# Kernel optimization log

Measured on AMD Instinct MI355X. Metric: run time of the kernel, lower is better.

## Reference

```python
import jax, jax.numpy as jnp
import numpy as np

NUM_EXPERTS = 4
TOPK = 1
TEMPERATURE = 1.0
NORM_TOPK_PROB = True
N_CLS = 1
N_REL = 4


def setup_inputs() -> dict:
    key = jax.random.key(0)
    ks = jax.random.split(key, 7)
    B, N_total, D, r, E = 64, 1029, 768, 64, NUM_EXPERTS
    x = jax.random.normal(ks[0], (B, N_total, D), dtype=jnp.float32)
    # parameters (torch Linear convention: weight [out, in])
    Wd = jax.random.normal(ks[1], (r, D), dtype=jnp.float32) * (1.0 / np.sqrt(D))
    Wg = jax.random.normal(ks[2], (E, r), dtype=jnp.float32) * (1.0 / np.sqrt(r))
    We = jax.random.normal(ks[3], (E, r, r), dtype=jnp.float32) * (1.0 / np.sqrt(r))
    be = jax.random.normal(ks[4], (E, r), dtype=jnp.float32) * 0.01
    Wu = jax.random.normal(ks[5], (D, r), dtype=jnp.float32) * (1.0 / np.sqrt(r))
    gamma = jnp.ones((D,), dtype=jnp.float32)  # LayerScale init_values=1.0
    return {"x": x, "Wd": Wd, "Wg": Wg, "We": We, "be": be, "Wu": Wu, "gamma": gamma}


def reference(x, Wd, Wg, We, be, Wu, gamma):
    # proj_down (bias=False) + exact GELU (nn.GELU default)
    h = jax.nn.gelu(jnp.einsum('bnd,rd->bnr', x, Wd), approximate=False)  # [B,Nt,r]
    cls_tok = h[:, :N_CLS, :]
    rel_tok = h[:, N_CLS:N_CLS + N_REL, :]
    t = h[:, N_CLS + N_REL:, :]                                           # [B,N,r]
    B, N, r = t.shape

    # gating: softmax scores, top-k selection
    logits = jnp.einsum('bnr,er->bne', t, Wg) / TEMPERATURE
    scores = jax.nn.softmax(logits, axis=-1)                              # [B,N,E]
    topk_w, topk_idx = jax.lax.top_k(scores, TOPK)                        # [B,N,K]
    if TOPK > 1 and NORM_TOPK_PROB:
        topk_w = topk_w / jnp.sum(topk_w, axis=-1, keepdims=True)

    # experts are tiny Linear(r,r): compute all experts densely, then gather.
    # Same math as per-expert gather/GEMM/scatter-combine in the source.
    expert_all = jnp.einsum('bnr,esr->bnes', t, We) + be                  # [B,N,E,r]
    idx_b = jnp.broadcast_to(topk_idx[..., None], (B, N, TOPK, r))
    sel = jnp.take_along_axis(expert_all, idx_b, axis=2)                  # [B,N,K,r]
    combine = jnp.sum(sel * topk_w[..., None], axis=2)                    # [B,N,r]

    full = jnp.concatenate([cls_tok, rel_tok, t + combine], axis=1)       # [B,Nt,r]
    # proj_up (bias=False) + LayerScale
    return jnp.einsum('bnr,dr->bnd', full, Wu) * gamma
```

## Files before the change

kernel.cpp:

```cpp
#include <hip/hip_runtime.h>
#include <math.h>


#define GELU(v) (0.5f*(v)*(1.0f + erff((v)*0.70710678118654752440f)))

__global__ __launch_bounds__(256) void k1_proj_gelu(
    const float* __restrict__ x, const float* __restrict__ Wd,
    float* __restrict__ h)
{
    __shared__ float As[64][68];
    __shared__ float Bs[64][68];
    const int tid = threadIdx.x;
    const int bm  = blockIdx.x;
    const int tm4 = (tid >> 4) << 2;
    const int tn4 = (tid & 15) << 2;
    const float* xblk = x + (size_t)bm * 64 * 768;

    float acc[4][4];
    #pragma unroll
    for (int i = 0; i < 4; ++i)
        #pragma unroll
        for (int j = 0; j < 4; ++j) acc[i][j] = 0.f;

    for (int kt = 0; kt < 768; kt += 64) {
        #pragma unroll
        for (int p = 0; p < 4; ++p) {
            int li = p*1024 + tid*4;
            int m = li >> 6, k = li & 63;
            float4 v = *(const float4*)(xblk + m*768 + kt + k);
            *(float4*)&As[m][k] = v;
        }
        #pragma unroll
        for (int p = 0; p < 4; ++p) {
            int li = p*1024 + tid*4;
            int j = li >> 6, k = li & 63;
            float4 v = *(const float4*)(Wd + j*768 + kt + k);
            int c = j ^ (((k >> 2) & 7) << 2);
            Bs[k+0][c] = v.x; Bs[k+1][c] = v.y; Bs[k+2][c] = v.z; Bs[k+3][c] = v.w;
        }
        __syncthreads();
        #pragma unroll
        for (int kk = 0; kk < 64; kk += 4) {
            const int swz = ((kk >> 2) & 7) << 2;
            float4 av[4], bv[4];
            #pragma unroll
            for (int i = 0; i < 4; ++i) av[i] = *(const float4*)&As[tm4 + i][kk];
            #pragma unroll
            for (int r = 0; r < 4; ++r) bv[r] = *(const float4*)&Bs[kk + r][tn4 ^ swz];
            #pragma unroll
            for (int i = 0; i < 4; ++i) {
                acc[i][0] += av[i].x*bv[0].x; acc[i][1] += av[i].x*bv[0].y;
                acc[i][2] += av[i].x*bv[0].z; acc[i][3] += av[i].x*bv[0].w;
                acc[i][0] += av[i].y*bv[1].x; acc[i][1] += av[i].y*bv[1].y;
                acc[i][2] += av[i].y*bv[1].z; acc[i][3] += av[i].y*bv[1].w;
                acc[i][0] += av[i].z*bv[2].x; acc[i][1] += av[i].z*bv[2].y;
                acc[i][2] += av[i].z*bv[2].z; acc[i][3] += av[i].z*bv[2].w;
                acc[i][0] += av[i].w*bv[3].x; acc[i][1] += av[i].w*bv[3].y;
                acc[i][2] += av[i].w*bv[3].z; acc[i][3] += av[i].w*bv[3].w;
            }
        }
        __syncthreads();
    }
    #pragma unroll
    for (int i = 0; i < 4; ++i) {
        int token = bm*64 + tm4 + i;
        float4 o;
        o.x = GELU(acc[i][0]); o.y = GELU(acc[i][1]);
        o.z = GELU(acc[i][2]); o.w = GELU(acc[i][3]);
        *(float4*)(h + (size_t)token*64 + tn4) = o;
    }
}

__global__ __launch_bounds__(256) void k2_moe(
    const float* __restrict__ Wg, const float* __restrict__ We,
    const float* __restrict__ be, float* __restrict__ h)
{
    __shared__ float sWg[4*64];
    __shared__ float sBe[4*64];
    __shared__ float sWeT[4*64*65];
    __shared__ float sT[4][64];
    const int tid = threadIdx.x;

    for (int i = tid; i < 4*64; i += 256) { sWg[i] = Wg[i]; sBe[i] = be[i]; }
    for (int i = tid; i < 4*64*64; i += 256) {
        int e = i >> 12, rem = i & 4095, s = rem >> 6, k = rem & 63;
        sWeT[(e*64 + k)*65 + s] = We[i];
    }
    __syncthreads();

    const int wv = tid >> 6, lane = tid & 63;
    #pragma unroll 1
    for (int it = 0; it < 16; ++it) {
        int mt = blockIdx.x*64 + wv*16 + it;
        int b = mt >> 10, n = mt & 1023;
        int token = b*1029 + 5 + n;
        float t = h[(size_t)token*64 + lane];

        float l0 = t * sWg[      lane];
        float l1 = t * sWg[ 64 + lane];
        float l2 = t * sWg[128 + lane];
        float l3 = t * sWg[192 + lane];
        #pragma unroll
        for (int off = 32; off > 0; off >>= 1) {
            l0 += __shfl_xor(l0, off);
            l1 += __shfl_xor(l1, off);
            l2 += __shfl_xor(l2, off);
            l3 += __shfl_xor(l3, off);
        }
        int ei = 0; float lm = l0;
        if (l1 > lm) { lm = l1; ei = 1; }
        if (l2 > lm) { lm = l2; ei = 2; }
        if (l3 > lm) { lm = l3; ei = 3; }
        float s = expf(l0 - lm) + expf(l1 - lm) + expf(l2 - lm) + expf(l3 - lm);
        float w = 1.0f / s;

        sT[wv][lane] = t;
        float o = sBe[ei*64 + lane];
        const float* wp = &sWeT[(ei*64)*65 + lane];
        #pragma unroll 8
        for (int k = 0; k < 64; ++k)
            o += sT[wv][k] * wp[k*65];

        h[(size_t)token*64 + lane] = t + w * o;
    }
}

__global__ __launch_bounds__(256) void k3_up_gamma(
    const float* __restrict__ h, const float* __restrict__ Wu,
    const float* __restrict__ gamma, float* __restrict__ out)
{
    __shared__ float Fs[64][68];
    __shared__ float Ws[64][132];
    const int tid = threadIdx.x;
    const int bm = blockIdx.x, bn = blockIdx.y;
    const int tm4 = (tid >> 4) << 2;
    const int tn8 = (tid & 15) << 3;

    #pragma unroll
    for (int p = 0; p < 4; ++p) {
        int li = p*1024 + tid*4;
        int m = li >> 6, k = li & 63;
        *(float4*)&Fs[m][k] = *(const float4*)(h + (size_t)(bm*64 + m)*64 + k);
    }
    #pragma unroll
    for (int p = 0; p < 8; ++p) {
        int li = p*1024 + tid*4;
        int dl = li >> 6, k = li & 63;
        float4 v = *(const float4*)(Wu + (size_t)(bn*128 + dl)*64 + k);
        int c = dl ^ (((k >> 2) & 7) << 2);
        Ws[k+0][c] = v.x; Ws[k+1][c] = v.y; Ws[k+2][c] = v.z; Ws[k+3][c] = v.w;
    }
    __syncthreads();

    float acc[4][8];
    #pragma unroll
    for (int i = 0; i < 4; ++i)
        #pragma unroll
        for (int j = 0; j < 8; ++j) acc[i][j] = 0.f;

    #pragma unroll
    for (int kk = 0; kk < 64; kk += 4) {
        const int swz = ((kk >> 2) & 7) << 2;
        float4 av[4], blo[4], bhi[4];
        #pragma unroll
        for (int i = 0; i < 4; ++i) av[i] = *(const float4*)&Fs[tm4 + i][kk];
        #pragma unroll
        for (int r = 0; r < 4; ++r) {
            blo[r] = *(const float4*)&Ws[kk + r][ tn8      ^ swz];
            bhi[r] = *(const float4*)&Ws[kk + r][(tn8 + 4) ^ swz];
        }
        #pragma unroll
        for (int i = 0; i < 4; ++i) {
            float a0 = av[i].x, a1 = av[i].y, a2 = av[i].z, a3 = av[i].w;
            acc[i][0] += a0*blo[0].x; acc[i][1] += a0*blo[0].y; acc[i][2] += a0*blo[0].z; acc[i][3] += a0*blo[0].w;
            acc[i][4] += a0*bhi[0].x; acc[i][5] += a0*bhi[0].y; acc[i][6] += a0*bhi[0].z; acc[i][7] += a0*bhi[0].w;
            acc[i][0] += a1*blo[1].x; acc[i][1] += a1*blo[1].y; acc[i][2] += a1*blo[1].z; acc[i][3] += a1*blo[1].w;
            acc[i][4] += a1*bhi[1].x; acc[i][5] += a1*bhi[1].y; acc[i][6] += a1*bhi[1].z; acc[i][7] += a1*bhi[1].w;
            acc[i][0] += a2*blo[2].x; acc[i][1] += a2*blo[2].y; acc[i][2] += a2*blo[2].z; acc[i][3] += a2*blo[2].w;
            acc[i][4] += a2*bhi[2].x; acc[i][5] += a2*bhi[2].y; acc[i][6] += a2*bhi[2].z; acc[i][7] += a2*bhi[2].w;
            acc[i][0] += a3*blo[3].x; acc[i][1] += a3*blo[3].y; acc[i][2] += a3*blo[3].z; acc[i][3] += a3*blo[3].w;
            acc[i][4] += a3*bhi[3].x; acc[i][5] += a3*bhi[3].y; acc[i][6] += a3*bhi[3].z; acc[i][7] += a3*bhi[3].w;
        }
    }

    float4 g0 = *(const float4*)(gamma + bn*128 + tn8);
    float4 g1 = *(const float4*)(gamma + bn*128 + tn8 + 4);
    #pragma unroll
    for (int i = 0; i < 4; ++i) {
        int token = bm*64 + tm4 + i;
        float4 o0, o1;
        o0.x = acc[i][0]*g0.x; o0.y = acc[i][1]*g0.y; o0.z = acc[i][2]*g0.z; o0.w = acc[i][3]*g0.w;
        o1.x = acc[i][4]*g1.x; o1.y = acc[i][5]*g1.y; o1.z = acc[i][6]*g1.z; o1.w = acc[i][7]*g1.w;
        float* op = out + (size_t)token*768 + bn*128 + tn8;
        *(float4*)op       = o0;
        *(float4*)(op + 4) = o1;
    }
}

extern "C" void kernel_launch(void* const* d_in, const int* in_sizes, int n_in,
                              void* d_out, int out_size, void* d_ws, size_t ws_size,
                              hipStream_t stream) {
    const float* x     = (const float*)d_in[0];
    const float* Wd    = (const float*)d_in[1];
    const float* Wg    = (const float*)d_in[2];
    const float* We    = (const float*)d_in[3];
    const float* be    = (const float*)d_in[4];
    const float* Wu    = (const float*)d_in[5];
    const float* gamma = (const float*)d_in[6];
    float* out = (float*)d_out;
    float* h   = (float*)d_ws;

    k1_proj_gelu<<<1029, 256, 0, stream>>>(x, Wd, h);
    k2_moe<<<1024, 256, 0, stream>>>(Wg, We, be, h);
    k3_up_gamma<<<dim3(1029, 6), 256, 0, stream>>>(h, Wu, gamma, out);
}
```

Before: 530.7 us.

## Fuse MoE and up-projection into one bf16 MFMA kernel, double-buffer down-projection

The MoE expert stage and the up-projection now run in a single kernel per 64-token tile. Expert and up-projection weights are pre-converted to bf16 and multiplied with MFMA instructions, so the intermediate no longer makes a second round trip through global memory. The down-projection kernel switches to a 32-wide K tile with register prefetch of the next tile and a higher occupancy hint. Using bf16 for the expert and up-projection matmuls lowers precision versus the fp32 reference. Computing all four experts densely and then selecting one adds MFMA work.

```diff
diff --git a/kernel.cpp b/kernel.cpp
--- a/kernel.cpp
+++ b/kernel.cpp
@@ -4,12 +4,28 @@
 
 #define GELU(v) (0.5f*(v)*(1.0f + erff((v)*0.70710678118654752440f)))
 
-__global__ __launch_bounds__(256) void k1_proj_gelu(
+typedef __attribute__((ext_vector_type(8))) short short8;
+typedef __attribute__((ext_vector_type(4))) float f32x4;
+
+__device__ __forceinline__ short f2bf(float f) {
+    union { float f; unsigned u; } c; c.f = f;
+    unsigned u = c.u;
+    return (short)((u + 0x7fffu + ((u >> 16) & 1u)) >> 16);
+}
+
+__global__ void k0_prep(const float* __restrict__ We, const float* __restrict__ Wu,
+                        short* __restrict__ WeB, short* __restrict__ WuB) {
+    int i = blockIdx.x * 256 + threadIdx.x;
+    if (i < 16384)       WeB[i] = f2bf(We[i]);
+    else if (i < 65536)  WuB[i - 16384] = f2bf(Wu[i - 16384]);
+}
+
+__global__ __launch_bounds__(256, 6) void k1_proj_gelu(
     const float* __restrict__ x, const float* __restrict__ Wd,
     float* __restrict__ h)
 {
-    __shared__ float As[64][68];
-    __shared__ float Bs[64][68];
+    __shared__ float As[64][36];
+    __shared__ float Bs[32][68];
     const int tid = threadIdx.x;
     const int bm  = blockIdx.x;
     const int tm4 = (tid >> 4) << 2;
@@ -22,31 +38,38 @@
         #pragma unroll
         for (int j = 0; j < 4; ++j) acc[i][j] = 0.f;
 
-    for (int kt = 0; kt < 768; kt += 64) {
-        #pragma unroll
-        for (int p = 0; p < 4; ++p) {
-            int li = p*1024 + tid*4;
-            int m = li >> 6, k = li & 63;
-            float4 v = *(const float4*)(xblk + m*768 + kt + k);
-            *(float4*)&As[m][k] = v;
-        }
-        #pragma unroll
-        for (int p = 0; p < 4; ++p) {
-            int li = p*1024 + tid*4;
-            int j = li >> 6, k = li & 63;
-            float4 v = *(const float4*)(Wd + j*768 + kt + k);
-            int c = j ^ (((k >> 2) & 7) << 2);
-            Bs[k+0][c] = v.x; Bs[k+1][c] = v.y; Bs[k+2][c] = v.z; Bs[k+3][c] = v.w;
-        }
-        __syncthreads();
-        #pragma unroll
-        for (int kk = 0; kk < 64; kk += 4) {
+    #pragma unroll
+    for (int p = 0; p < 2; ++p) {
+        int li = p*1024 + tid*4;
+        int m = li >> 5, k = li & 31;
+        *(f32x4*)&As[m][k] = *(const f32x4*)(xblk + m*768 + k);
+        int j = m;
+        f32x4 v = *(const f32x4*)(Wd + j*768 + k);
+        int c = j ^ (((k >> 2) & 7) << 2);
+        Bs[k+0][c] = v.x; Bs[k+1][c] = v.y; Bs[k+2][c] = v.z; Bs[k+3][c] = v.w;
+    }
+    __syncthreads();
+
+    for (int kt = 0; kt < 768; kt += 32) {
+        const bool more = (kt + 32) < 768;
+        f32x4 nxa[2], nxb[2];
+        if (more) {
+            #pragma unroll
+            for (int p = 0; p < 2; ++p) {
+                int li = p*1024 + tid*4;
+                int m = li >> 5, k = li & 31;
+                nxa[p] = *(const f32x4*)(xblk + m*768 + kt + 32 + k);
+                nxb[p] = *(const f32x4*)(Wd  + m*768 + kt + 32 + k);
+            }
+        }
+        #pragma unroll
+        for (int kk = 0; kk < 32; kk += 4) {
             const int swz = ((kk >> 2) & 7) << 2;
-            float4 av[4], bv[4];
-            #pragma unroll
-            for (int i = 0; i < 4; ++i) av[i] = *(const float4*)&As[tm4 + i][kk];
-            #pragma unroll
-            for (int r = 0; r < 4; ++r) bv[r] = *(const float4*)&Bs[kk + r][tn4 ^ swz];
+            f32x4 av[4], bv[4];
+            #pragma unroll
+            for (int i = 0; i < 4; ++i) av[i] = *(const f32x4*)&As[tm4 + i][kk];
+            #pragma unroll
+            for (int r = 0; r < 4; ++r) bv[r] = *(const f32x4*)&Bs[kk + r][tn4 ^ swz];
             #pragma unroll
             for (int i = 0; i < 4; ++i) {
                 acc[i][0] += av[i].x*bv[0].x; acc[i][1] += av[i].x*bv[0].y;
@@ -60,140 +83,154 @@
             }
         }
         __syncthreads();
+        if (more) {
+            #pragma unroll
+            for (int p = 0; p < 2; ++p) {
+                int li = p*1024 + tid*4;
+                int m = li >> 5, k = li & 31;
+                *(f32x4*)&As[m][k] = nxa[p];
+                int c = m ^ (((k >> 2) & 7) << 2);
+                Bs[k+0][c] = nxb[p].x; Bs[k+1][c] = nxb[p].y;
+                Bs[k+2][c] = nxb[p].z; Bs[k+3][c] = nxb[p].w;
+            }
+            __syncthreads();
+        }
     }
     #pragma unroll
     for (int i = 0; i < 4; ++i) {
         int token = bm*64 + tm4 + i;
-        float4 o;
+        f32x4 o;
         o.x = GELU(acc[i][0]); o.y = GELU(acc[i][1]);
         o.z = GELU(acc[i][2]); o.w = GELU(acc[i][3]);
-        *(float4*)(h + (size_t)token*64 + tn4) = o;
-    }
-}
-
-__global__ __launch_bounds__(256) void k2_moe(
-    const float* __restrict__ Wg, const float* __restrict__ We,
-    const float* __restrict__ be, float* __restrict__ h)
+        *(f32x4*)(h + (size_t)token*64 + tn4) = o;
+    }
+}
+
+__global__ __launch_bounds__(256, 4) void k23_moe_up(
+    const float* __restrict__ h, const short* __restrict__ WeB,
+    const short* __restrict__ WuB, const float* __restrict__ Wg,
+    const float* __restrict__ be, const float* __restrict__ gamma,
+    float* __restrict__ out)
 {
-    __shared__ float sWg[4*64];
-    __shared__ float sBe[4*64];
-    __shared__ float sWeT[4*64*65];
-    __shared__ float sT[4][64];
+    __shared__ float hS[64][68];
+    __shared__ float sWg[4][68];
+    __shared__ float sBe[4][68];
+    __shared__ float sGm[768];
+    __shared__ float sLg[64][5];
+    __shared__ float sW[64];
+    __shared__ int   sEi[64];
+
     const int tid = threadIdx.x;
-
-    for (int i = tid; i < 4*64; i += 256) { sWg[i] = Wg[i]; sBe[i] = be[i]; }
-    for (int i = tid; i < 4*64*64; i += 256) {
-        int e = i >> 12, rem = i & 4095, s = rem >> 6, k = rem & 63;
-        sWeT[(e*64 + k)*65 + s] = We[i];
-    }
-    __syncthreads();
-
-    const int wv = tid >> 6, lane = tid & 63;
-    #pragma unroll 1
-    for (int it = 0; it < 16; ++it) {
-        int mt = blockIdx.x*64 + wv*16 + it;
-        int b = mt >> 10, n = mt & 1023;
-        int token = b*1029 + 5 + n;
-        float t = h[(size_t)token*64 + lane];
-
-        float l0 = t * sWg[      lane];
-        float l1 = t * sWg[ 64 + lane];
-        float l2 = t * sWg[128 + lane];
-        float l3 = t * sWg[192 + lane];
-        #pragma unroll
-        for (int off = 32; off > 0; off >>= 1) {
-            l0 += __shfl_xor(l0, off);
-            l1 += __shfl_xor(l1, off);
-            l2 += __shfl_xor(l2, off);
-            l3 += __shfl_xor(l3, off);
-        }
+    const int tb  = blockIdx.x * 64;
+
+    #pragma unroll
+    for (int p = 0; p < 4; ++p) {
+        int li = p*1024 + tid*4;
+        int m = li >> 6, k = li & 63;
+        *(f32x4*)&hS[m][k] = *(const f32x4*)(h + (size_t)(tb + m)*64 + k);
+    }
+    { int e = tid >> 6, k = tid & 63;
+      sWg[e][k] = Wg[tid]; sBe[e][k] = be[tid]; }
+    for (int i = tid; i < 768; i += 256) sGm[i] = gamma[i];
+    __syncthreads();
+
+    {
+        int tok = tid >> 2, e = tid & 3;
+        float s = 0.f;
+        #pragma unroll 8
+        for (int k = 0; k < 64; ++k) s += hS[tok][k] * sWg[e][k];
+        sLg[tok][e] = s;
+    }
+    __syncthreads();
+    if (tid < 64) {
+        float l0 = sLg[tid][0], l1 = sLg[tid][1], l2 = sLg[tid][2], l3 = sLg[tid][3];
         int ei = 0; float lm = l0;
         if (l1 > lm) { lm = l1; ei = 1; }
         if (l2 > lm) { lm = l2; ei = 2; }
         if (l3 > lm) { lm = l3; ei = 3; }
-        float s = expf(l0 - lm) + expf(l1 - lm) + expf(l2 - lm) + expf(l3 - lm);
-        float w = 1.0f / s;
-
-        sT[wv][lane] = t;
-        float o = sBe[ei*64 + lane];
-        const float* wp = &sWeT[(ei*64)*65 + lane];
-        #pragma unroll 8
-        for (int k = 0; k < 64; ++k)
-            o += sT[wv][k] * wp[k*65];
-
-        h[(size_t)token*64 + lane] = t + w * o;
-    }
-}
-
-__global__ __launch_bounds__(256) void k3_up_gamma(
-    const float* __restrict__ h, const float* __restrict__ Wu,
-    const float* __restrict__ gamma, float* __restrict__ out)
-{
-    __shared__ float Fs[64][68];
-    __shared__ float Ws[64][132];
-    const int tid = threadIdx.x;
-    const int bm = blockIdx.x, bn = blockIdx.y;
-    const int tm4 = (tid >> 4) << 2;
-    const int tn8 = (tid & 15) << 3;
-
-    #pragma unroll
-    for (int p = 0; p < 4; ++p) {
-        int li = p*1024 + tid*4;
-        int m = li >> 6, k = li & 63;
-        *(float4*)&Fs[m][k] = *(const float4*)(h + (size_t)(bm*64 + m)*64 + k);
-    }
-    #pragma unroll
-    for (int p = 0; p < 8; ++p) {
-        int li = p*1024 + tid*4;
-        int dl = li >> 6, k = li & 63;
-        float4 v = *(const float4*)(Wu + (size_t)(bn*128 + dl)*64 + k);
-        int c = dl ^ (((k >> 2) & 7) << 2);
-        Ws[k+0][c] = v.x; Ws[k+1][c] = v.y; Ws[k+2][c] = v.z; Ws[k+3][c] = v.w;
-    }
-    __syncthreads();
-
-    float acc[4][8];
-    #pragma unroll
-    for (int i = 0; i < 4; ++i)
-        #pragma unroll
-        for (int j = 0; j < 8; ++j) acc[i][j] = 0.f;
-
-    #pragma unroll
-    for (int kk = 0; kk < 64; kk += 4) {
-        const int swz = ((kk >> 2) & 7) << 2;
-        float4 av[4], blo[4], bhi[4];
-        #pragma unroll
-        for (int i = 0; i < 4; ++i) av[i] = *(const float4*)&Fs[tm4 + i][kk];
-        #pragma unroll
-        for (int r = 0; r < 4; ++r) {
-            blo[r] = *(const float4*)&Ws[kk + r][ tn8      ^ swz];
-            bhi[r] = *(const float4*)&Ws[kk + r][(tn8 + 4) ^ swz];
-        }
-        #pragma unroll
-        for (int i = 0; i < 4; ++i) {
-            float a0 = av[i].x, a1 = av[i].y, a2 = av[i].z, a3 = av[i].w;
-            acc[i][0] += a0*blo[0].x; acc[i][1] += a0*blo[0].y; acc[i][2] += a0*blo[0].z; acc[i][3] += a0*blo[0].w;
-            acc[i][4] += a0*bhi[0].x; acc[i][5] += a0*bhi[0].y; acc[i][6] += a0*bhi[0].z; acc[i][7] += a0*bhi[0].w;
-            acc[i][0] += a1*blo[1].x; acc[i][1] += a1*blo[1].y; acc[i][2] += a1*blo[1].z; acc[i][3] += a1*blo[1].w;
-            acc[i][4] += a1*bhi[1].x; acc[i][5] += a1*bhi[1].y; acc[i][6] += a1*bhi[1].z; acc[i][7] += a1*bhi[1].w;
-            acc[i][0] += a2*blo[2].x; acc[i][1] += a2*blo[2].y; acc[i][2] += a2*blo[2].z; acc[i][3] += a2*blo[2].w;
-            acc[i][4] += a2*bhi[2].x; acc[i][5] += a2*bhi[2].y; acc[i][6] += a2*bhi[2].z; acc[i][7] += a2*bhi[2].w;
-            acc[i][0] += a3*blo[3].x; acc[i][1] += a3*blo[3].y; acc[i][2] += a3*blo[3].z; acc[i][3] += a3*blo[3].w;
-            acc[i][4] += a3*bhi[3].x; acc[i][5] += a3*bhi[3].y; acc[i][6] += a3*bhi[3].z; acc[i][7] += a3*bhi[3].w;
-        }
-    }
-
-    float4 g0 = *(const float4*)(gamma + bn*128 + tn8);
-    float4 g1 = *(const float4*)(gamma + bn*128 + tn8 + 4);
-    #pragma unroll
-    for (int i = 0; i < 4; ++i) {
-        int token = bm*64 + tm4 + i;
-        float4 o0, o1;
-        o0.x = acc[i][0]*g0.x; o0.y = acc[i][1]*g0.y; o0.z = acc[i][2]*g0.z; o0.w = acc[i][3]*g0.w;
-        o1.x = acc[i][4]*g1.x; o1.y = acc[i][5]*g1.y; o1.z = acc[i][6]*g1.z; o1.w = acc[i][7]*g1.w;
-        float* op = out + (size_t)token*768 + bn*128 + tn8;
-        *(float4*)op       = o0;
-        *(float4*)(op + 4) = o1;
+        float s = expf(l0-lm) + expf(l1-lm) + expf(l2-lm) + expf(l3-lm);
+        unsigned token = tb + tid;
+        unsigned pos = token % 1029u;
+        sW[tid]  = (pos < 5u) ? 0.f : (1.f / s);
+        sEi[tid] = ei;
+    }
+    __syncthreads();
+
+    const int wv = tid >> 6, lane = tid & 63;
+    const int q = lane >> 4, c = lane & 15;
+    const int r0 = wv * 16;
+
+    short8 af[2];
+    #pragma unroll
+    for (int ks = 0; ks < 2; ++ks) {
+        const float* p = &hS[r0 + c][ks*32 + q*8];
+        f32x4 v0 = *(const f32x4*)p, v1 = *(const f32x4*)(p + 4);
+        short8 a;
+        a[0]=f2bf(v0.x); a[1]=f2bf(v0.y); a[2]=f2bf(v0.z); a[3]=f2bf(v0.w);
+        a[4]=f2bf(v1.x); a[5]=f2bf(v1.y); a[6]=f2bf(v1.z); a[7]=f2bf(v1.w);
+        af[ks] = a;
+    }
+
+    f32x4 eacc[4][4];
+    #pragma unroll
+    for (int e = 0; e < 4; ++e)
+        #pragma unroll
+        for (int st = 0; st < 4; ++st) {
+            f32x4 acc = {0.f, 0.f, 0.f, 0.f};
+            #pragma unroll
+            for (int ks = 0; ks < 2; ++ks) {
+                short8 b = *(const short8*)(WeB + ((e*64 + st*16 + c)*64 + ks*32 + q*8));
+                acc = __builtin_amdgcn_mfma_f32_16x16x32_bf16(af[ks], b, acc, 0, 0, 0);
+            }
+            eacc[e][st] = acc;
+        }
+
+    float wq[4]; int eq[4];
+    #pragma unroll
+    for (int reg = 0; reg < 4; ++reg) {
+        int row = r0 + q*4 + reg;
+        wq[reg] = sW[row]; eq[reg] = sEi[row];
+    }
+    float tv[4][4];
+    #pragma unroll
+    for (int st = 0; st < 4; ++st)
+        #pragma unroll
+        for (int reg = 0; reg < 4; ++reg)
+            tv[st][reg] = hS[r0 + q*4 + reg][st*16 + c];
+    #pragma unroll
+    for (int st = 0; st < 4; ++st)
+        #pragma unroll
+        for (int reg = 0; reg < 4; ++reg) {
+            int ei = eq[reg];
+            float ea = (ei == 0) ? eacc[0][st][reg] :
+                       (ei == 1) ? eacc[1][st][reg] :
+                       (ei == 2) ? eacc[2][st][reg] : eacc[3][st][reg];
+            float bev = sBe[ei][st*16 + c];
+            hS[r0 + q*4 + reg][st*16 + c] = tv[st][reg] + wq[reg]*(ea + bev);
+        }
+    __syncthreads();
+
+    short8 af2[2];
+    #pragma unroll
+    for (int ks = 0; ks < 2; ++ks) {
+        const float* p = &hS[r0 + c][ks*32 + q*8];
+        f32x4 v0 = *(const f32x4*)p, v1 = *(const f32x4*)(p + 4);
+        short8 a;
+        a[0]=f2bf(v0.x); a[1]=f2bf(v0.y); a[2]=f2bf(v0.z); a[3]=f2bf(v0.w);
+        a[4]=f2bf(v1.x); a[5]=f2bf(v1.y); a[6]=f2bf(v1.z); a[7]=f2bf(v1.w);
+        af2[ks] = a;
+    }
+    #pragma unroll 4
+    for (int nt = 0; nt < 48; ++nt) {
+        f32x4 acc = {0.f, 0.f, 0.f, 0.f};
+        short8 b0 = *(const short8*)(WuB + ((nt*16 + c)*64 + q*8));
+        short8 b1 = *(const short8*)(WuB + ((nt*16 + c)*64 + 32 + q*8));
+        acc = __builtin_amdgcn_mfma_f32_16x16x32_bf16(af2[0], b0, acc, 0, 0, 0);
+        acc = __builtin_amdgcn_mfma_f32_16x16x32_bf16(af2[1], b1, acc, 0, 0, 0);
+        float g = sGm[nt*16 + c];
+        #pragma unroll
+        for (int reg = 0; reg < 4; ++reg)
+            out[(size_t)(tb + r0 + q*4 + reg)*768 + nt*16 + c] = acc[reg] * g;
     }
 }
 
@@ -208,9 +245,12 @@
     const float* Wu    = (const float*)d_in[5];
     const float* gamma = (const float*)d_in[6];
     float* out = (float*)d_out;
-    float* h   = (float*)d_ws;
-
+
+    short* WeB = (short*)d_ws;
+    short* WuB = (short*)d_ws + 16384;
+    float* h   = (float*)((char*)d_ws + 131072);
+
+    k0_prep<<<256, 256, 0, stream>>>(We, Wu, WeB, WuB);
     k1_proj_gelu<<<1029, 256, 0, stream>>>(x, Wd, h);
-    k2_moe<<<1024, 256, 0, stream>>>(Wg, We, be, h);
-    k3_up_gamma<<<dim3(1029, 6), 256, 0, stream>>>(h, Wu, gamma, out);
-}
+    k23_moe_up<<<1029, 256, 0, stream>>>(h, WeB, WuB, Wg, be, gamma, out);
+}
```

After: 648.5 us. +22.2%, slower.
